# Kernel tuning notes

Measured on AMD Instinct MI355X. Metric: run time of the kernel, lower is better.

The kernel has to match this reference:

```python
import jax, jax.numpy as jnp
import numpy as np
from jax import lax

N_HEAD, D_IN, D_HID, D_OUT = 8, 64, 64, 64
SEQ = 32768
STD = 1.0 / np.sqrt(D_HID * N_HEAD)


def _unif(key, shape):
    return jax.random.uniform(key, shape, jnp.float32, -STD, STD)


def setup_inputs() -> dict:
    key = jax.random.key(0)
    ks = jax.random.split(key, 12)
    D = N_HEAD * D_IN
    return {
        "inputs": jax.random.normal(ks[0], (SEQ, D), jnp.float32),
        "W_in": _unif(ks[1], (D, D)),
        "b_in": _unif(ks[2], (D,)),
        "W_gates": _unif(ks[3], (D_IN, 3 * D_HID)),
        "b_gates": _unif(ks[4], (3 * D_HID,)),
        "W_og": _unif(ks[5], (D_IN, D_HID)),
        "b_og": _unif(ks[6], (D_HID,)),
        "W_c": _unif(ks[7], (D_HID, D_OUT)),
        "b_c": _unif(ks[8], (D_OUT,)),
        "W_out": _unif(ks[9], (N_HEAD * D_OUT, N_HEAD * D_OUT)),
        "b_out": _unif(ks[10], (N_HEAD * D_OUT,)),
    }


def reference(inputs, W_in, b_in, W_gates, b_gates, W_og, b_og, W_c, b_c, W_out, b_out):
    S = inputs.shape[0]
    # input mixing across heads, then flatten: (S, H*d_in) -> (S*H, d_in)
    x = (inputs @ W_in + b_in).reshape(S * N_HEAD, D_IN)
    # FirstModule: fused gate projection
    g = x @ W_gates + b_gates  # (S*H, 3*d_hid)
    fg = jax.nn.sigmoid(g[:, :D_HID])
    ig = jax.nn.sigmoid(g[:, D_HID:2 * D_HID])
    h = jnp.tanh(g[:, 2 * D_HID:])
    hr = ig * h
    # linear recurrence c_t = fg_t * c_{t-1} + hr_t, c_0 = 0, via associative scan
    def comb(e1, e2):
        a1, b1 = e1
        a2, b2 = e2
        return (a1 * a2, b1 * a2 + b2)
    _, c = lax.associative_scan(comb, (fg, hr))  # (S*H, d_hid)
    # SecondModule: output gate and projection
    og = jax.nn.sigmoid(x @ W_og + b_og)
    o = (og * c) @ W_c + b_c  # (S*H, d_out)
    o = o.reshape(S, N_HEAD * D_OUT)
    return o @ W_out + b_out
```

## Files before the change

kernel.cpp:

```cpp
#include <hip/hip_runtime.h>


typedef unsigned short ushort;
typedef __bf16 bf16x8 __attribute__((ext_vector_type(8)));
typedef float f32x4 __attribute__((ext_vector_type(4)));

#define CROWS 64
#define NCH  4096
#define NSUP 64

#define GLOAD16(gp, lp) __builtin_amdgcn_global_load_lds( \
    (const __attribute__((address_space(1))) void*)(gp),  \
    (__attribute__((address_space(3))) void*)(lp), 16, 0, 0)

__device__ inline float b2f(ushort u) {
    return __builtin_bit_cast(float, (unsigned)u << 16);
}
__device__ inline ushort f2b(float f) {
    unsigned x = __builtin_bit_cast(unsigned, f);
    x += 0x7FFFu + ((x >> 16) & 1u);
    return (ushort)(x >> 16);
}

__global__ void transpose512(const float* __restrict__ src, ushort* __restrict__ dst) {
    __shared__ float tile[32][33];
    const int tx = threadIdx.x & 31, ty = threadIdx.x >> 5;
    const int x0 = blockIdx.x * 32, y0 = blockIdx.y * 32;
    #pragma unroll
    for (int dy = 0; dy < 32; dy += 8)
        tile[ty + dy][tx] = src[(size_t)(y0 + ty + dy) * 512 + x0 + tx];
    __syncthreads();
    #pragma unroll
    for (int dy = 0; dy < 32; dy += 8)
        dst[(size_t)(x0 + ty + dy) * 512 + y0 + tx] = f2b(tile[tx][ty + dy]);
}

__global__ void prep_small(const float* __restrict__ W_gates, const float* __restrict__ W_og,
                           const float* __restrict__ W_c,
                           const float* __restrict__ b_gates, const float* __restrict__ b_og,
                           ushort* __restrict__ W2T, ushort* __restrict__ WcT, float* __restrict__ b2) {
    const int idx = blockIdx.x * 256 + threadIdx.x;
    if (idx < 16384) {
        const int n = idx >> 6, k = idx & 63;
        W2T[idx] = f2b((n < 192) ? W_gates[k * 192 + n] : W_og[(k << 6) + (n - 192)]);
    } else if (idx < 16384 + 4096) {
        const int i = idx - 16384;
        const int n = i >> 6, k = i & 63;
        WcT[i] = f2b(W_c[(k << 6) + n]);
    } else if (idx < 16384 + 4096 + 256) {
        const int i = idx - 20480;
        b2[i] = (i < 192) ? b_gates[i] : b_og[i - 192];
    }
}

template <int BM, int BN, int WAVES_M, int WAVES_N, int A32, int C32>
__global__ __launch_bounds__(256)
void gemm_bt(const void* __restrict__ Av, const ushort* __restrict__ Bt,
             const float* __restrict__ bias, void* __restrict__ Cv,
             int M, int N, int K) {
    constexpr int WM = BM / WAVES_M, WN = BN / WAVES_N;
    constexpr int MT = WM / 16, NT = WN / 16;
    __shared__ __align__(16) ushort sA[BM * 32];
    __shared__ __align__(16) ushort sB[BN * 32];

    const int t = threadIdx.x, w = t >> 6, lane = t & 63;
    const int wm = (w / WAVES_N) * WM, wn = (w % WAVES_N) * WN;
    const long bm = (long)blockIdx.x * BM, bn = (long)blockIdx.y * BN;

    f32x4 acc[MT][NT] = {};

    for (int k0 = 0; k0 < K; k0 += 32) {
        if (A32) {
            const float* A = (const float*)Av;
            #pragma unroll
            for (int is = 0; is < BM / 32; ++is) {
                const int row = is * 32 + (t >> 3), col = (t & 7) * 4;
                const float4 v = *(const float4*)(A + (bm + row) * (long)K + k0 + col);
                *(ushort4*)&sA[row * 32 + col] =
                    make_ushort4(f2b(v.x), f2b(v.y), f2b(v.z), f2b(v.w));
            }
        } else {
            const ushort* A = (const ushort*)Av;
            #pragma unroll
            for (int is = 0; is < BM / 64; ++is)
                GLOAD16(A + (bm + is * 64 + (t >> 2)) * (long)K + k0 + (t & 3) * 8,
                        (char*)sA + is * 4096 + w * 1024);
        }
        #pragma unroll
        for (int is = 0; is < BN / 64; ++is)
            GLOAD16(Bt + (bn + is * 64 + (t >> 2)) * (long)K + k0 + (t & 3) * 8,
                    (char*)sB + is * 4096 + w * 1024);
        __syncthreads();

        bf16x8 af[MT], bfr[NT];
        #pragma unroll
        for (int i = 0; i < MT; ++i)
            af[i] = *(const bf16x8*)&sA[(wm + i * 16 + (lane & 15)) * 32 + (lane >> 4) * 8];
        #pragma unroll
        for (int j = 0; j < NT; ++j)
            bfr[j] = *(const bf16x8*)&sB[(wn + j * 16 + (lane & 15)) * 32 + (lane >> 4) * 8];
        #pragma unroll
        for (int i = 0; i < MT; ++i)
            #pragma unroll
            for (int j = 0; j < NT; ++j)
                acc[i][j] = __builtin_amdgcn_mfma_f32_16x16x32_bf16(af[i], bfr[j], acc[i][j], 0, 0, 0);
        __syncthreads();
    }

    #pragma unroll
    for (int i = 0; i < MT; ++i)
        #pragma unroll
        for (int j = 0; j < NT; ++j) {
            const long col = bn + wn + j * 16 + (lane & 15);
            const float bv = bias[col];
            #pragma unroll
            for (int r = 0; r < 4; ++r) {
                const long row = bm + wm + i * 16 + ((lane >> 4) << 2) + r;
                const float v = acc[i][j][r] + bv;
                if (C32) ((float*)Cv)[row * (long)N + col] = v;
                else     ((ushort*)Cv)[row * (long)N + col] = f2b(v);
            }
        }
}

template <int APPLY>
__global__ __launch_bounds__(256)
void gates_scan(const ushort* __restrict__ X, const ushort* __restrict__ W2T,
                const float* __restrict__ b2, const ushort* __restrict__ WcT,
                const float* __restrict__ b_c,
                float* __restrict__ Agg, float* __restrict__ Bgg,
                const float* __restrict__ PreS, ushort* __restrict__ O) {
    __shared__ __align__(16) char smem[46080];
    ushort* sA = (ushort*)smem;
    ushort* sB = (ushort*)(smem + 8192);
    ushort* sG = (ushort*)smem;
    ushort* sP = (ushort*)(smem + 36864);
    __shared__ __align__(16) ushort sWc[64 * 64];

    const int t = threadIdx.x, w = t >> 6, lane = t & 63;
    const int blk = blockIdx.x;
    const long row0 = (long)blk * CROWS;

    #pragma unroll
    for (int is = 0; is < 2; ++is)
        GLOAD16(X + (row0 + is * 32 + (t >> 3)) * 64 + (t & 7) * 8,
                (char*)sA + is * 4096 + w * 1024);
    #pragma unroll
    for (int is = 0; is < 8; ++is)
        GLOAD16(W2T + (is * 32 + (t >> 3)) * 64 + (t & 7) * 8,
                (char*)sB + is * 4096 + w * 1024);
    if (APPLY) {
        #pragma unroll
        for (int is = 0; is < 2; ++is)
            GLOAD16(WcT + (is * 32 + (t >> 3)) * 64 + (t & 7) * 8,
                    (char*)sWc + is * 4096 + w * 1024);
    }
    __syncthreads();

    const int wm = (w >> 1) * 32, wn = (w & 1) * 128;
    f32x4 acc[2][8] = {};
    #pragma unroll
    for (int kk = 0; kk < 2; ++kk) {
        bf16x8 af[2], bfr[8];
        #pragma unroll
        for (int i = 0; i < 2; ++i)
            af[i] = *(const bf16x8*)&sA[(wm + i * 16 + (lane & 15)) * 64 + kk * 32 + (lane >> 4) * 8];
        #pragma unroll
        for (int j = 0; j < 8; ++j)
            bfr[j] = *(const bf16x8*)&sB[(wn + j * 16 + (lane & 15)) * 64 + kk * 32 + (lane >> 4) * 8];
        #pragma unroll
        for (int i = 0; i < 2; ++i)
            #pragma unroll
            for (int j = 0; j < 8; ++j)
                acc[i][j] = __builtin_amdgcn_mfma_f32_16x16x32_bf16(af[i], bfr[j], acc[i][j], 0, 0, 0);
    }
    __syncthreads();

    #pragma unroll
    for (int j = 0; j < 8; ++j) {
        const int col = wn + j * 16 + (lane & 15);
        const float bv = b2[col];
        const int g = col >> 6, ch = col & 63;
        #pragma unroll
        for (int i = 0; i < 2; ++i)
            #pragma unroll
            for (int r = 0; r < 4; ++r) {
                const int row = wm + i * 16 + ((lane >> 4) << 2) + r;
                float v = acc[i][j][r] + bv;
                v = (g == 2) ? tanhf(v) : 1.0f / (1.0f + __expf(-v));
                sG[g * 4608 + row * 72 + ch] = f2b(v);
            }
    }
    __syncthreads();

    if (!APPLY) {
        if (t < 64) {
            float a = 1.0f, b = 0.0f;
            #pragma unroll 8
            for (int r = 0; r < CROWS; ++r) {
                const float fg = b2f(sG[r * 72 + t]);
                const float hr = b2f(sG[4608 + r * 72 + t]) * b2f(sG[9216 + r * 72 + t]);
                a *= fg;
                b = fmaf(b, fg, hr);
            }
            Agg[blk * 64 + t] = a;
            Bgg[blk * 64 + t] = b;
        }
        return;
    }

    if (t < 64) {
        const int s = blk >> 6;
        float c = fmaf(PreS[s * 64 + t], Agg[blk * 64 + t], Bgg[blk * 64 + t]);
        #pragma unroll 8
        for (int r = 0; r < CROWS; ++r) {
            const float fg = b2f(sG[r * 72 + t]);
            const float hr = b2f(sG[4608 + r * 72 + t]) * b2f(sG[9216 + r * 72 + t]);
            c = fmaf(c, fg, hr);
            sP[r * 72 + t] = f2b(b2f(sG[13824 + r * 72 + t]) * c);
        }
    }
    __syncthreads();

    const int wm2 = (w >> 1) * 32, wn2 = (w & 1) * 32;
    f32x4 acc2[2][2] = {};
    #pragma unroll
    for (int kk = 0; kk < 2; ++kk) {
        bf16x8 pa[2], wb[2];
        #pragma unroll
        for (int i = 0; i < 2; ++i)
            pa[i] = *(const bf16x8*)&sP[(wm2 + i * 16 + (lane & 15)) * 72 + kk * 32 + (lane >> 4) * 8];
        #pragma unroll
        for (int j = 0; j < 2; ++j)
            wb[j] = *(const bf16x8*)&sWc[(wn2 + j * 16 + (lane & 15)) * 64 + kk * 32 + (lane >> 4) * 8];
        #pragma unroll
        for (int i = 0; i < 2; ++i)
            #pragma unroll
            for (int j = 0; j < 2; ++j)
                acc2[i][j] = __builtin_amdgcn_mfma_f32_16x16x32_bf16(pa[i], wb[j], acc2[i][j], 0, 0, 0);
    }
    #pragma unroll
    for (int i = 0; i < 2; ++i)
        #pragma unroll
        for (int j = 0; j < 2; ++j) {
            const int col = wn2 + j * 16 + (lane & 15);
            const float bv = b_c[col];
            #pragma unroll
            for (int r = 0; r < 4; ++r) {
                const int row = wm2 + i * 16 + ((lane >> 4) << 2) + r;
                O[(row0 + row) * 64 + col] = f2b(acc2[i][j][r] + bv);
            }
        }
}

__global__ void scan_super(float* __restrict__ Agg, float* __restrict__ Bgg,
                           float* __restrict__ SA, float* __restrict__ SB) {
    const int s = blockIdx.x, ch = threadIdx.x;
    float a = 1.0f, b = 0.0f;
    for (int j = 0; j < 64; ++j) {
        const int idx = (s * 64 + j) * 64 + ch;
        const float a2 = Agg[idx], bb = Bgg[idx];
        Agg[idx] = a;
        Bgg[idx] = b;
        a *= a2;
        b = fmaf(b, a2, bb);
    }
    SA[s * 64 + ch] = a;
    SB[s * 64 + ch] = b;
}

__global__ void scan_top(const float* __restrict__ SA, const float* __restrict__ SB,
                         float* __restrict__ PreS) {
    const int ch = threadIdx.x;
    float c = 0.0f;
    for (int s = 0; s < 64; ++s) {
        PreS[s * 64 + ch] = c;
        c = fmaf(c, SA[s * 64 + ch], SB[s * 64 + ch]);
    }
}

extern "C" void kernel_launch(void* const* d_in, const int* in_sizes, int n_in,
                              void* d_out, int out_size, void* d_ws, size_t ws_size,
                              hipStream_t stream) {
    const float* inputs  = (const float*)d_in[0];
    const float* W_in    = (const float*)d_in[1];
    const float* b_in    = (const float*)d_in[2];
    const float* W_gates = (const float*)d_in[3];
    const float* b_gates = (const float*)d_in[4];
    const float* W_og    = (const float*)d_in[5];
    const float* b_og    = (const float*)d_in[6];
    const float* W_c     = (const float*)d_in[7];
    const float* b_c     = (const float*)d_in[8];
    const float* W_out   = (const float*)d_in[9];
    const float* b_out   = (const float*)d_in[10];
    float* out = (float*)d_out;

    char* ws = (char*)d_ws;
    ushort* X     = (ushort*)(ws);
    ushort* WinT  = (ushort*)(ws + 33554432);
    ushort* WoutT = (ushort*)(ws + 34078720);
    ushort* W2T   = (ushort*)(ws + 34603008);
    ushort* WcT   = (ushort*)(ws + 34635776);
    float*  b2    = (float*)(ws + 34643968);
    float*  Agg   = (float*)(ws + 34644992);
    float*  Bgg   = (float*)(ws + 35693568);
    float*  SA    = (float*)(ws + 36742144);
    float*  SB    = (float*)(ws + 36758528);
    float*  PreS  = (float*)(ws + 36774912);
    ushort* O = X;

    transpose512<<<dim3(16, 16), 256, 0, stream>>>(W_in, WinT);
    transpose512<<<dim3(16, 16), 256, 0, stream>>>(W_out, WoutT);
    prep_small<<<81, 256, 0, stream>>>(W_gates, W_og, W_c, b_gates, b_og, W2T, WcT, b2);

    gemm_bt<128, 128, 2, 2, 1, 0><<<dim3(256, 4), 256, 0, stream>>>(
        inputs, WinT, b_in, X, 32768, 512, 512);

    gates_scan<0><<<NCH, 256, 0, stream>>>(X, W2T, b2, WcT, b_c, Agg, Bgg, PreS, O);
    scan_super<<<NSUP, 64, 0, stream>>>(Agg, Bgg, SA, SB);
    scan_top<<<1, 64, 0, stream>>>(SA, SB, PreS);
    gates_scan<1><<<NCH, 256, 0, stream>>>(X, W2T, b2, WcT, b_c, Agg, Bgg, PreS, O);

    gemm_bt<128, 128, 2, 2, 0, 1><<<dim3(256, 4), 256, 0, stream>>>(
        O, WoutT, b_out, out, 32768, 512, 512);
}
```

Before: 354.3 us.

## Swizzle LDS layouts, reorder gate columns to fuse ig*tanh, use fast tanh

Applies XOR swizzling to the LDS tiles in the GEMM and gates_scan kernels to reduce bank conflicts on the MFMA operand reads. The gate weight columns are reordered to [ig, h, fg, og] so each wave pair computes ig*tanh(h) in registers and stores one hr tile instead of separate ig and h tiles, which shrinks shared memory and the scan's LDS reads. It replaces tanhf with an exp-based approximation and skips computing og in the non-apply pass. It also adds unroll pragmas to the small scan kernels. The fast tanh may lose some accuracy, and the swizzle index math adds a few integer ops.

```diff
diff --git a/kernel.cpp b/kernel.cpp
--- a/kernel.cpp
+++ b/kernel.cpp
@@ -21,6 +21,8 @@
     x += 0x7FFFu + ((x >> 16) & 1u);
     return (ushort)(x >> 16);
 }
+__device__ inline float sigm(float v) { return 1.0f / (1.0f + __expf(-v)); }
+__device__ inline float tanh_fast(float v) { return 2.0f / (1.0f + __expf(-2.0f * v)) - 1.0f; }
 
 __global__ void transpose512(const float* __restrict__ src, ushort* __restrict__ dst) {
     __shared__ float tile[32][33];
@@ -42,14 +44,24 @@
     const int idx = blockIdx.x * 256 + threadIdx.x;
     if (idx < 16384) {
         const int n = idx >> 6, k = idx & 63;
-        W2T[idx] = f2b((n < 192) ? W_gates[k * 192 + n] : W_og[(k << 6) + (n - 192)]);
+        float v;
+        if      (n < 64)  v = W_gates[k * 192 + 64 + n];
+        else if (n < 128) v = W_gates[k * 192 + 128 + (n - 64)];
+        else if (n < 192) v = W_gates[k * 192 + (n - 128)];
+        else              v = W_og[k * 64 + (n - 192)];
+        W2T[idx] = f2b(v);
     } else if (idx < 16384 + 4096) {
         const int i = idx - 16384;
         const int n = i >> 6, k = i & 63;
         WcT[i] = f2b(W_c[(k << 6) + n]);
     } else if (idx < 16384 + 4096 + 256) {
         const int i = idx - 20480;
-        b2[i] = (i < 192) ? b_gates[i] : b_og[i - 192];
+        float v;
+        if      (i < 64)  v = b_gates[64 + i];
+        else if (i < 128) v = b_gates[128 + (i - 64)];
+        else if (i < 192) v = b_gates[i - 128];
+        else              v = b_og[i - 192];
+        b2[i] = v;
     }
 }
 
@@ -74,31 +86,40 @@
             const float* A = (const float*)Av;
             #pragma unroll
             for (int is = 0; is < BM / 32; ++is) {
-                const int row = is * 32 + (t >> 3), col = (t & 7) * 4;
-                const float4 v = *(const float4*)(A + (bm + row) * (long)K + k0 + col);
-                *(ushort4*)&sA[row * 32 + col] =
+                const int row = is * 32 + (t >> 3);
+                const int cd = (t & 7) >> 1, half = t & 1;
+                const float4 v = *(const float4*)(A + (bm + row) * (long)K + k0 + (t & 7) * 4);
+                *(ushort4*)&sA[row * 32 + ((cd ^ (row & 3)) * 8) + half * 4] =
                     make_ushort4(f2b(v.x), f2b(v.y), f2b(v.z), f2b(v.w));
             }
         } else {
             const ushort* A = (const ushort*)Av;
             #pragma unroll
-            for (int is = 0; is < BM / 64; ++is)
-                GLOAD16(A + (bm + is * 64 + (t >> 2)) * (long)K + k0 + (t & 3) * 8,
+            for (int is = 0; is < BM / 64; ++is) {
+                const int row = t >> 2, kc = t & 3;
+                GLOAD16(A + (bm + is * 64 + row) * (long)K + k0 + ((kc ^ (row & 3)) * 8),
                         (char*)sA + is * 4096 + w * 1024);
-        }
-        #pragma unroll
-        for (int is = 0; is < BN / 64; ++is)
-            GLOAD16(Bt + (bn + is * 64 + (t >> 2)) * (long)K + k0 + (t & 3) * 8,
+            }
+        }
+        #pragma unroll
+        for (int is = 0; is < BN / 64; ++is) {
+            const int row = t >> 2, kc = t & 3;
+            GLOAD16(Bt + (bn + is * 64 + row) * (long)K + k0 + ((kc ^ (row & 3)) * 8),
                     (char*)sB + is * 4096 + w * 1024);
+        }
         __syncthreads();
 
         bf16x8 af[MT], bfr[NT];
         #pragma unroll
-        for (int i = 0; i < MT; ++i)
-            af[i] = *(const bf16x8*)&sA[(wm + i * 16 + (lane & 15)) * 32 + (lane >> 4) * 8];
-        #pragma unroll
-        for (int j = 0; j < NT; ++j)
-            bfr[j] = *(const bf16x8*)&sB[(wn + j * 16 + (lane & 15)) * 32 + (lane >> 4) * 8];
+        for (int i = 0; i < MT; ++i) {
+            const int row = wm + i * 16 + (lane & 15), c = lane >> 4;
+            af[i] = *(const bf16x8*)&sA[row * 32 + ((c ^ (row & 3)) * 8)];
+        }
+        #pragma unroll
+        for (int j = 0; j < NT; ++j) {
+            const int rb = wn + j * 16 + (lane & 15), c = lane >> 4;
+            bfr[j] = *(const bf16x8*)&sB[rb * 32 + ((c ^ (rb & 3)) * 8)];
+        }
         #pragma unroll
         for (int i = 0; i < MT; ++i)
             #pragma unroll
@@ -130,66 +151,90 @@
                 const float* __restrict__ b_c,
                 float* __restrict__ Agg, float* __restrict__ Bgg,
                 const float* __restrict__ PreS, ushort* __restrict__ O) {
-    __shared__ __align__(16) char smem[46080];
-    ushort* sA = (ushort*)smem;
-    ushort* sB = (ushort*)(smem + 8192);
-    ushort* sG = (ushort*)smem;
-    ushort* sP = (ushort*)(smem + 36864);
-    __shared__ __align__(16) ushort sWc[64 * 64];
+    __shared__ __align__(16) char smem[40960];
+    ushort* sA  = (ushort*)smem;
+    ushort* sB  = (ushort*)(smem + 8192);
+    ushort* sFG = (ushort*)smem;
+    ushort* sHR = (ushort*)(smem + 9216);
+    ushort* sOG = (ushort*)(smem + 18432);
+    ushort* sP  = (ushort*)(smem + 27648);
+    __shared__ __align__(16) ushort sWc[4096];
 
     const int t = threadIdx.x, w = t >> 6, lane = t & 63;
     const int blk = blockIdx.x;
     const long row0 = (long)blk * CROWS;
 
-    #pragma unroll
-    for (int is = 0; is < 2; ++is)
-        GLOAD16(X + (row0 + is * 32 + (t >> 3)) * 64 + (t & 7) * 8,
-                (char*)sA + is * 4096 + w * 1024);
-    #pragma unroll
-    for (int is = 0; is < 8; ++is)
-        GLOAD16(W2T + (is * 32 + (t >> 3)) * 64 + (t & 7) * 8,
-                (char*)sB + is * 4096 + w * 1024);
-    if (APPLY) {
+    {
+        const int row = t >> 3, kc = t & 7;
         #pragma unroll
         for (int is = 0; is < 2; ++is)
-            GLOAD16(WcT + (is * 32 + (t >> 3)) * 64 + (t & 7) * 8,
-                    (char*)sWc + is * 4096 + w * 1024);
-    }
-    __syncthreads();
-
-    const int wm = (w >> 1) * 32, wn = (w & 1) * 128;
+            GLOAD16(X + (row0 + is * 32 + row) * 64 + ((kc ^ (row & 7)) * 8),
+                    (char*)sA + is * 4096 + w * 1024);
+        #pragma unroll
+        for (int is = 0; is < 8; ++is)
+            GLOAD16(W2T + (is * 32 + row) * 64 + ((kc ^ (row & 7)) * 8),
+                    (char*)sB + is * 4096 + w * 1024);
+        if (APPLY) {
+            #pragma unroll
+            for (int is = 0; is < 2; ++is)
+                GLOAD16(WcT + (is * 32 + row) * 64 + ((kc ^ (row & 7)) * 8),
+                        (char*)sWc + is * 4096 + w * 1024);
+        }
+    }
+    __syncthreads();
+
+    const int wm = (w >> 1) * 32;
+    const int grpB = w & 1;
+    const int colbase = grpB * 128;
     f32x4 acc[2][8] = {};
     #pragma unroll
     for (int kk = 0; kk < 2; ++kk) {
-        bf16x8 af[2], bfr[8];
-        #pragma unroll
-        for (int i = 0; i < 2; ++i)
-            af[i] = *(const bf16x8*)&sA[(wm + i * 16 + (lane & 15)) * 64 + kk * 32 + (lane >> 4) * 8];
-        #pragma unroll
-        for (int j = 0; j < 8; ++j)
-            bfr[j] = *(const bf16x8*)&sB[(wn + j * 16 + (lane & 15)) * 64 + kk * 32 + (lane >> 4) * 8];
-        #pragma unroll
-        for (int i = 0; i < 2; ++i)
-            #pragma unroll
-            for (int j = 0; j < 8; ++j)
-                acc[i][j] = __builtin_amdgcn_mfma_f32_16x16x32_bf16(af[i], bfr[j], acc[i][j], 0, 0, 0);
-    }
-    __syncthreads();
-
-    #pragma unroll
-    for (int j = 0; j < 8; ++j) {
-        const int col = wn + j * 16 + (lane & 15);
-        const float bv = b2[col];
-        const int g = col >> 6, ch = col & 63;
-        #pragma unroll
-        for (int i = 0; i < 2; ++i)
-            #pragma unroll
-            for (int r = 0; r < 4; ++r) {
-                const int row = wm + i * 16 + ((lane >> 4) << 2) + r;
-                float v = acc[i][j][r] + bv;
-                v = (g == 2) ? tanhf(v) : 1.0f / (1.0f + __expf(-v));
-                sG[g * 4608 + row * 72 + ch] = f2b(v);
-            }
+        bf16x8 af[2];
+        #pragma unroll
+        for (int i = 0; i < 2; ++i) {
+            const int row = wm + i * 16 + (lane & 15), c = kk * 4 + (lane >> 4);
+            af[i] = *(const bf16x8*)&sA[row * 64 + ((c ^ (row & 7)) * 8)];
+        }
+        #pragma unroll
+        for (int j = 0; j < 8; ++j) {
+            const int rb = colbase + j * 16 + (lane & 15), c = kk * 4 + (lane >> 4);
+            const bf16x8 bf = *(const bf16x8*)&sB[rb * 64 + ((c ^ (rb & 7)) * 8)];
+            #pragma unroll
+            for (int i = 0; i < 2; ++i)
+                acc[i][j] = __builtin_amdgcn_mfma_f32_16x16x32_bf16(af[i], bf, acc[i][j], 0, 0, 0);
+        }
+    }
+    __syncthreads();
+
+    if (!grpB) {
+        #pragma unroll
+        for (int jj = 0; jj < 4; ++jj) {
+            const int ch = jj * 16 + (lane & 15);
+            const float bi = b2[ch], bh = b2[64 + ch];
+            #pragma unroll
+            for (int i = 0; i < 2; ++i)
+                #pragma unroll
+                for (int r = 0; r < 4; ++r) {
+                    const int row = wm + i * 16 + ((lane >> 4) << 2) + r;
+                    const float gi = acc[i][jj][r] + bi;
+                    const float gh = acc[i][jj + 4][r] + bh;
+                    sHR[row * 72 + ch] = f2b(sigm(gi) * tanh_fast(gh));
+                }
+        }
+    } else {
+        #pragma unroll
+        for (int jj = 0; jj < 4; ++jj) {
+            const int ch = jj * 16 + (lane & 15);
+            const float bfg = b2[128 + ch], bog = b2[192 + ch];
+            #pragma unroll
+            for (int i = 0; i < 2; ++i)
+                #pragma unroll
+                for (int r = 0; r < 4; ++r) {
+                    const int row = wm + i * 16 + ((lane >> 4) << 2) + r;
+                    sFG[row * 72 + ch] = f2b(sigm(acc[i][jj][r] + bfg));
+                    if (APPLY) sOG[row * 72 + ch] = f2b(sigm(acc[i][jj + 4][r] + bog));
+                }
+        }
     }
     __syncthreads();
 
@@ -198,8 +243,8 @@
             float a = 1.0f, b = 0.0f;
             #pragma unroll 8
             for (int r = 0; r < CROWS; ++r) {
-                const float fg = b2f(sG[r * 72 + t]);
-                const float hr = b2f(sG[4608 + r * 72 + t]) * b2f(sG[9216 + r * 72 + t]);
+                const float fg = b2f(sFG[r * 72 + t]);
+                const float hr = b2f(sHR[r * 72 + t]);
                 a *= fg;
                 b = fmaf(b, fg, hr);
             }
@@ -210,14 +255,14 @@
     }
 
     if (t < 64) {
-        const int s = blk >> 6;
-        float c = fmaf(PreS[s * 64 + t], Agg[blk * 64 + t], Bgg[blk * 64 + t]);
+        float c = fmaf(PreS[(blk >> 6) * 64 + t], Agg[blk * 64 + t], Bgg[blk * 64 + t]);
+        const int cch = t >> 3, half = t & 7;
         #pragma unroll 8
         for (int r = 0; r < CROWS; ++r) {
-            const float fg = b2f(sG[r * 72 + t]);
-            const float hr = b2f(sG[4608 + r * 72 + t]) * b2f(sG[9216 + r * 72 + t]);
+            const float fg = b2f(sFG[r * 72 + t]);
+            const float hr = b2f(sHR[r * 72 + t]);
             c = fmaf(c, fg, hr);
-            sP[r * 72 + t] = f2b(b2f(sG[13824 + r * 72 + t]) * c);
+            sP[r * 64 + ((cch ^ (r & 7)) * 8) + half] = f2b(b2f(sOG[r * 72 + t]) * c);
         }
     }
     __syncthreads();
@@ -228,11 +273,15 @@
     for (int kk = 0; kk < 2; ++kk) {
         bf16x8 pa[2], wb[2];
         #pragma unroll
-        for (int i = 0; i < 2; ++i)
-            pa[i] = *(const bf16x8*)&sP[(wm2 + i * 16 + (lane & 15)) * 72 + kk * 32 + (lane >> 4) * 8];
-        #pragma unroll
-        for (int j = 0; j < 2; ++j)
-            wb[j] = *(const bf16x8*)&sWc[(wn2 + j * 16 + (lane & 15)) * 64 + kk * 32 + (lane >> 4) * 8];
+        for (int i = 0; i < 2; ++i) {
+            const int row = wm2 + i * 16 + (lane & 15), c = kk * 4 + (lane >> 4);
+            pa[i] = *(const bf16x8*)&sP[row * 64 + ((c ^ (row & 7)) * 8)];
+        }
+        #pragma unroll
+        for (int j = 0; j < 2; ++j) {
+            const int rb = wn2 + j * 16 + (lane & 15), c = kk * 4 + (lane >> 4);
+            wb[j] = *(const bf16x8*)&sWc[rb * 64 + ((c ^ (rb & 7)) * 8)];
+        }
         #pragma unroll
         for (int i = 0; i < 2; ++i)
             #pragma unroll
@@ -257,6 +306,7 @@
                            float* __restrict__ SA, float* __restrict__ SB) {
     const int s = blockIdx.x, ch = threadIdx.x;
     float a = 1.0f, b = 0.0f;
+    #pragma unroll 8
     for (int j = 0; j < 64; ++j) {
         const int idx = (s * 64 + j) * 64 + ch;
         const float a2 = Agg[idx], bb = Bgg[idx];
@@ -273,6 +323,7 @@
                          float* __restrict__ PreS) {
     const int ch = threadIdx.x;
     float c = 0.0f;
+    #pragma unroll 8
     for (int s = 0; s < 64; ++s) {
         PreS[s * 64 + ch] = c;
         c = fmaf(c, SA[s * 64 + ch], SB[s * 64 + ch]);
```

Measured after the change: 324.6 us. 1.09x faster.
